# Optimization experiments

Measured on AMD Instinct MI355X. Metric: run time of the kernel, lower is better.

## Reference

```python
import jax, jax.numpy as jnp
import numpy as np

D_MODEL = 768
EXPAND = 2
D_INNER = EXPAND * D_MODEL  # 1536
D_STATE = 16
D_CONV = 4
DT_RANK = D_MODEL // 16  # 48
N_LAYER = 3
BATCH, SEQLEN = 2, 1024
EPS = 1e-5


def setup_inputs() -> dict:
    key = jax.random.key(0)
    ks = jax.random.split(key, 8)
    s = 0.02
    hidden_states = jax.random.normal(ks[0], (BATCH, SEQLEN, D_MODEL), jnp.float32)
    norm_w = jnp.ones((N_LAYER, D_MODEL), jnp.float32)
    in_proj_w = s * jax.random.normal(ks[1], (N_LAYER, 2 * D_INNER, D_MODEL), jnp.float32)
    conv_w = s * jax.random.normal(ks[2], (N_LAYER, D_INNER, D_CONV), jnp.float32)
    conv_b = jnp.zeros((N_LAYER, D_INNER), jnp.float32)
    x_proj_w = s * jax.random.normal(ks[3], (N_LAYER, DT_RANK + 2 * D_STATE, D_INNER), jnp.float32)
    dt_proj_w = s * jax.random.normal(ks[4], (N_LAYER, D_INNER, DT_RANK), jnp.float32)
    dt_proj_b = jnp.full((N_LAYER, D_INNER), -4.6, jnp.float32)  # softplus ~ 0.01
    # S4D-real init: A_log = log(1..d_state), tiled over channels
    A_log = jnp.tile(jnp.log(jnp.arange(1, D_STATE + 1, dtype=jnp.float32))[None, None, :], (N_LAYER, D_INNER, 1))
    D_skip = jnp.ones((N_LAYER, D_INNER), jnp.float32)
    out_proj_w = s * jax.random.normal(ks[5], (N_LAYER, D_MODEL, D_INNER), jnp.float32)
    norm_f_w = jnp.ones((D_MODEL,), jnp.float32)
    return dict(hidden_states=hidden_states, norm_w=norm_w, in_proj_w=in_proj_w,
                conv_w=conv_w, conv_b=conv_b, x_proj_w=x_proj_w, dt_proj_w=dt_proj_w,
                dt_proj_b=dt_proj_b, A_log=A_log, D_skip=D_skip, out_proj_w=out_proj_w,
                norm_f_w=norm_f_w)


def _rmsnorm(x, w):
    return x * jax.lax.rsqrt(jnp.mean(x * x, axis=-1, keepdims=True) + EPS) * w


def _causal_conv1d(x, w, b):
    # x: [B, L, D]; w: [D, K] depthwise; left-pad for causality
    xt = jnp.transpose(x, (0, 2, 1))  # [B, D, L]
    y = jax.lax.conv_general_dilated(xt, w[:, None, :], window_strides=(1,),
                                     padding=[(D_CONV - 1, 0)], feature_group_count=D_INNER)
    return jnp.transpose(y, (0, 2, 1)) + b


def _selective_scan(u, delta, A, Bc, Cc, Dp):
    # u, delta: [B, L, D]; A: [D, N]; Bc, Cc: [B, L, N]
    def step(h, inp):
        dt, bt, ct, ut = inp  # [B,D], [B,N], [B,N], [B,D]
        h = jnp.exp(dt[..., None] * A) * h + (dt * ut)[..., None] * bt[:, None, :]
        y = jnp.einsum('bdn,bn->bd', h, ct)
        return h, y
    h0 = jnp.zeros((u.shape[0], u.shape[2], A.shape[1]), u.dtype)
    xs = (jnp.swapaxes(delta, 0, 1), jnp.swapaxes(Bc, 0, 1), jnp.swapaxes(Cc, 0, 1), jnp.swapaxes(u, 0, 1))
    _, ys = jax.lax.scan(step, h0, xs)  # ys: [L, B, D]
    return jnp.swapaxes(ys, 0, 1) + u * Dp


def _mixer(h, in_w, cw, cb, xw, dtw, dtb, A_log, Dp, ow):
    xz = jnp.einsum('bld,ed->ble', h, in_w)  # [B, L, 2*D_INNER]
    x, z = xz[..., :D_INNER], xz[..., D_INNER:]
    x = jax.nn.silu(_causal_conv1d(x, cw, cb))
    x_dbl = jnp.einsum('bld,ed->ble', x, xw)
    dt = x_dbl[..., :DT_RANK]
    Bc = x_dbl[..., DT_RANK:DT_RANK + D_STATE]
    Cc = x_dbl[..., DT_RANK + D_STATE:]
    delta = jax.nn.softplus(jnp.einsum('blr,dr->bld', dt, dtw) + dtb)
    A = -jnp.exp(A_log)
    y = _selective_scan(x, delta, A, Bc, Cc, Dp)
    y = y * jax.nn.silu(z)
    return jnp.einsum('bld,ed->ble', y, ow)


def reference(hidden_states, norm_w, in_proj_w, conv_w, conv_b, x_proj_w, dt_proj_w,
              dt_proj_b, A_log, D_skip, out_proj_w, norm_f_w):
    hidden = hidden_states
    residual = None
    for i in range(N_LAYER):
        residual = hidden if residual is None else hidden + residual  # fused add
        hidden = _rmsnorm(residual, norm_w[i])
        hidden = _mixer(hidden, in_proj_w[i], conv_w[i], conv_b[i], x_proj_w[i],
                        dt_proj_w[i], dt_proj_b[i], A_log[i], D_skip[i], out_proj_w[i])
    # final fused add + RMSNorm (prenorm=False)
    return _rmsnorm(hidden + residual, norm_f_w)
```

## Files before the change

kernel.cpp:

```cpp
#include <hip/hip_runtime.h>
#include <math.h>

#define D_MODEL 768
#define D_INNER 1536
#define D_STATE 16
#define D_CONV 4
#define DT_RANK 48
#define N_LAYER 3
#define BATCH 2
#define SEQLEN 1024
#define NROWS (BATCH * SEQLEN)
#define XDBL_W (DT_RANK + 2 * D_STATE)
#define EPS 1e-5f

#define SCLEN 16
#define SDN 16
#define KSPLIT_X 8

typedef short bf16x8 __attribute__((ext_vector_type(8)));
typedef float f32x4 __attribute__((ext_vector_type(4)));

__device__ __forceinline__ ushort f2bf(float x) {
    union { float f; uint u; } v; v.f = x;
    uint r = v.u + 0x7fff + ((v.u >> 16) & 1);
    return (ushort)(r >> 16);
}

__device__ __forceinline__ void gload_lds16(const void* g, void* l) {
    __builtin_amdgcn_global_load_lds(
        (const __attribute__((address_space(1))) unsigned int*)g,
        (__attribute__((address_space(3))) unsigned int*)l, 16, 0, 0);
}

__global__ __launch_bounds__(256) void cvt_bf16_kernel(
    const float* __restrict__ s, ushort* __restrict__ d, int n4)
{
    int i = blockIdx.x * 256 + threadIdx.x;
    if (i >= n4) return;
    float4 v = ((const float4*)s)[i];
    ushort4 o;
    o.x = f2bf(v.x); o.y = f2bf(v.y); o.z = f2bf(v.z); o.w = f2bf(v.w);
    ((ushort4*)d)[i] = o;
}

__global__ __launch_bounds__(256) void cvt_xw_pad_kernel(
    const float* __restrict__ src, ushort* __restrict__ dst)
{
    const int per = 128 * 1536 / 4;
    int i = blockIdx.x * 256 + threadIdx.x;
    if (i >= 3 * per) return;
    int li = i / per, rem = i - li * per;
    int r = (rem * 4) / 1536, c = (rem * 4) % 1536;
    ushort4 o = make_ushort4(0, 0, 0, 0);
    if (r < XDBL_W) {
        const float* s = src + ((size_t)li * XDBL_W + r) * 1536 + c;
        o.x = f2bf(s[0]); o.y = f2bf(s[1]); o.z = f2bf(s[2]); o.w = f2bf(s[3]);
    }
    ((ushort4*)dst)[i] = o;
}

__global__ __launch_bounds__(256) void cvt_dtw_pad_kernel(
    const float* __restrict__ src, ushort* __restrict__ dst)
{
    const int per = 1536 * 64 / 4;
    int i = blockIdx.x * 256 + threadIdx.x;
    if (i >= 3 * per) return;
    int li = i / per, rem = i - li * per;
    int r = (rem * 4) / 64, c = (rem * 4) % 64;
    ushort4 o = make_ushort4(0, 0, 0, 0);
    if (c < DT_RANK) {
        const float* s = src + ((size_t)li * 1536 + r) * DT_RANK + c;
        o.x = f2bf(s[0]); o.y = f2bf(s[1]); o.z = f2bf(s[2]); o.w = f2bf(s[3]);
    }
    ((ushort4*)dst)[i] = o;
}

__global__ __launch_bounds__(256) void add_rmsnorm_kernel(
    const float* __restrict__ x, const float* __restrict__ res_in,
    const float* __restrict__ w, float* __restrict__ res_out,
    float* __restrict__ normed_f32, ushort* __restrict__ normed_bf)
{
    int row = blockIdx.x;
    int tid = threadIdx.x;
    const float* xr = x + row * D_MODEL;
    float v[3];
    float ss = 0.f;
#pragma unroll
    for (int i = 0; i < 3; i++) {
        int c = tid + i * 256;
        float t = xr[c];
        if (res_in) t += res_in[row * D_MODEL + c];
        v[i] = t;
        ss += t * t;
    }
    for (int off = 32; off; off >>= 1) ss += __shfl_xor(ss, off, 64);
    __shared__ float red[4];
    if ((tid & 63) == 0) red[tid >> 6] = ss;
    __syncthreads();
    float tot = red[0] + red[1] + red[2] + red[3];
    float scale = rsqrtf(tot * (1.f / D_MODEL) + EPS);
#pragma unroll
    for (int i = 0; i < 3; i++) {
        int c = tid + i * 256;
        if (res_out) res_out[row * D_MODEL + c] = v[i];
        float o = v[i] * scale * w[c];
        if (normed_f32) normed_f32[row * D_MODEL + c] = o;
        if (normed_bf)  normed_bf[row * D_MODEL + c] = f2bf(o);
    }
}

template <int BM, int BN, int EPI, int SPLITK>
__global__ __launch_bounds__(256) void gemm_mfma_kernel(
    const ushort* __restrict__ A, const ushort* __restrict__ W,
    const float* __restrict__ bias, float* __restrict__ C,
    int ldc, int Nout, int M, int K)
{
    constexpr int TM = BM / 32;
    constexpr int TN = BN / 32;
    __shared__ __attribute__((aligned(16))) ushort As[BM * 64];
    __shared__ __attribute__((aligned(16))) ushort Ws[BN * 64];
    const int t = threadIdx.x;
    const int lane = t & 63, w = t >> 6;
    const int ln15 = lane & 15, q = lane >> 4;
    const int row0 = blockIdx.y * BM, col0 = blockIdx.x * BN;
    const int wm0 = (w & 1) * (BM / 2), wn0 = (w >> 1) * (BN / 2);

    int kper = K / SPLITK;
    int kz = (SPLITK > 1) ? blockIdx.z * kper : 0;
    if (SPLITK > 1) C += (size_t)blockIdx.z * M * ldc;

    f32x4 acc[TM][TN];
#pragma unroll
    for (int i = 0; i < TM; i++)
#pragma unroll
        for (int j = 0; j < TN; j++) acc[i][j] = (f32x4){0.f, 0.f, 0.f, 0.f};

    for (int k0 = kz; k0 < kz + kper; k0 += 64) {
        __syncthreads();
#pragma unroll
        for (int i = 0; i < BM / 32; i++) {
            int p = (i * 4 + w) * 64 + lane;
            int r = p >> 3, s = p & 7;
            int g = s ^ (r & 7);
            gload_lds16(A + (size_t)(row0 + r) * K + k0 + g * 8, &As[p * 8]);
        }
#pragma unroll
        for (int i = 0; i < BN / 32; i++) {
            int p = (i * 4 + w) * 64 + lane;
            int r = p >> 3, s = p & 7;
            int g = s ^ (r & 7);
            gload_lds16(W + (size_t)(col0 + r) * K + k0 + g * 8, &Ws[p * 8]);
        }
        __syncthreads();
#pragma unroll
        for (int ks = 0; ks < 2; ks++) {
            bf16x8 af[TM], wf[TN];
#pragma unroll
            for (int im = 0; im < TM; im++) {
                int m = wm0 + im * 16 + ln15;
                int slot = (ks * 4 + q) ^ (m & 7);
                af[im] = *(const bf16x8*)&As[m * 64 + slot * 8];
            }
#pragma unroll
            for (int jn = 0; jn < TN; jn++) {
                int n = wn0 + jn * 16 + ln15;
                int slot = (ks * 4 + q) ^ (n & 7);
                wf[jn] = *(const bf16x8*)&Ws[n * 64 + slot * 8];
            }
#pragma unroll
            for (int im = 0; im < TM; im++)
#pragma unroll
                for (int jn = 0; jn < TN; jn++)
                    acc[im][jn] = __builtin_amdgcn_mfma_f32_16x16x32_bf16(
                        af[im], wf[jn], acc[im][jn], 0, 0, 0);
        }
    }
#pragma unroll
    for (int im = 0; im < TM; im++) {
#pragma unroll
        for (int jn = 0; jn < TN; jn++) {
            int rr = row0 + wm0 + im * 16 + q * 4;
            int cc = col0 + wn0 + jn * 16 + ln15;
            if (cc < Nout) {
                float* cp = C + (size_t)rr * ldc + cc;
#pragma unroll
                for (int r = 0; r < 4; r++) {
                    float v = acc[im][jn][r];
                    if (EPI == 1) {
                        v += bias[cc];
                        v = (v > 20.f) ? v : log1pf(__expf(v));
                    }
                    cp[(size_t)r * ldc] = v;
                }
            }
        }
    }
}

__global__ __launch_bounds__(256) void xreduce_kernel(
    const float* __restrict__ Cp, float* __restrict__ xdbl,
    ushort* __restrict__ xdt)
{
    const int S4 = NROWS * XDBL_W / 4;
    int i = blockIdx.x * 256 + threadIdx.x;
    if (i >= S4) return;
    const float4* p = (const float4*)Cp;
    float4 o = p[i];
#pragma unroll
    for (int z = 1; z < KSPLIT_X; z++) {
        float4 a = p[i + (size_t)z * S4];
        o.x += a.x; o.y += a.y; o.z += a.z; o.w += a.w;
    }
    ((float4*)xdbl)[i] = o;
    int row = (i * 4) / XDBL_W, c0 = (i * 4) % XDBL_W;
    if (c0 < DT_RANK) {
        ushort4 b;
        b.x = f2bf(o.x); b.y = f2bf(o.y); b.z = f2bf(o.z); b.w = f2bf(o.w);
        *(ushort4*)&xdt[(size_t)row * 64 + c0] = b;
    } else if (c0 < 64) {
        *(ushort4*)&xdt[(size_t)row * 64 + c0] = make_ushort4(0, 0, 0, 0);
    }
}

__global__ __launch_bounds__(256) void conv_silu_kernel(
    const float* __restrict__ xz, const float* __restrict__ cw,
    const float* __restrict__ cb, float* __restrict__ out,
    ushort* __restrict__ out_bf)
{
    int idx = blockIdx.x * 256 + threadIdx.x;
    int d = idx % D_INNER;
    int bl = idx / D_INNER;
    int l = bl % SEQLEN;
    float s = cb[d];
    const float* xp = xz + (size_t)bl * (2 * D_INNER) + d;
#pragma unroll
    for (int k = 0; k < D_CONV; k++) {
        int ls = l - (D_CONV - 1) + k;
        if (ls >= 0) s += cw[d * D_CONV + k] * xp[(k - (D_CONV - 1)) * (2 * D_INNER)];
    }
    float sil = s / (1.f + __expf(-s));
    out[(size_t)bl * D_INNER + d] = sil;
    out_bf[(size_t)bl * D_INNER + d] = f2bf(sil);
}

__global__ __launch_bounds__(1024) void scan2_kernel(
    const float* __restrict__ u, const float* __restrict__ delta,
    const float* __restrict__ A_log, const float* __restrict__ xdbl,
    const float* __restrict__ Dskip, const float* __restrict__ xz,
    ushort* __restrict__ ybf)
{
    __shared__ float PL[16][SDN * 17];
    __shared__ float HL[16][SDN * 17];
    const int t = threadIdx.x;
    const int lane = t & 63;
    const int w = t >> 6;
    const int dsub = lane & 15;
    const int csub = lane >> 4;
    const int c = w * 4 + csub;
    const int b = blockIdx.x / (D_INNER / SDN);
    const int d = (blockIdx.x % (D_INNER / SDN)) * SDN + dsub;

    float a2[D_STATE];
#pragma unroll
    for (int n = 0; n < D_STATE; n++)
        a2[n] = -__expf(A_log[d * D_STATE + n]) * 1.44269504f;

    const size_t base = (size_t)b * SEQLEN * D_INNER + d;
    const float* dtp = delta + base;
    const float* up  = u + base;
    const float* xrow = xdbl + (size_t)b * SEQLEN * XDBL_W;
    const int l0 = c * SCLEN;

    float h[D_STATE], P[D_STATE];
#pragma unroll
    for (int n = 0; n < D_STATE; n++) { h[n] = 0.f; P[n] = 1.f; }

    for (int i = 0; i < SCLEN; i++) {
        const int l = l0 + i;
        float dt = dtp[(size_t)l * D_INNER];
        float uu = up[(size_t)l * D_INNER];
        const float4* Bv = (const float4*)(xrow + (size_t)l * XDBL_W + DT_RANK);
        float4 q0 = Bv[0], q1 = Bv[1], q2 = Bv[2], q3 = Bv[3];
        float Bf[D_STATE] = {q0.x,q0.y,q0.z,q0.w, q1.x,q1.y,q1.z,q1.w,
                             q2.x,q2.y,q2.z,q2.w, q3.x,q3.y,q3.z,q3.w};
        float dtu = dt * uu;
#pragma unroll
        for (int n = 0; n < D_STATE; n++) {
            float e = __builtin_amdgcn_exp2f(dt * a2[n]);
            P[n] *= e;
            h[n] = e * h[n] + dtu * Bf[n];
        }
    }

#pragma unroll
    for (int n = 0; n < D_STATE; n++) {
        float Pp = __shfl(P[n], lane - 16, 64);
        float Hp = __shfl(h[n], lane - 16, 64);
        bool act = csub >= 1;
        h[n] = act ? P[n] * Hp + h[n] : h[n];
        P[n] = act ? P[n] * Pp : P[n];
    }
#pragma unroll
    for (int n = 0; n < D_STATE; n++) {
        float Pp = __shfl(P[n], lane - 32, 64);
        float Hp = __shfl(h[n], lane - 32, 64);
        bool act = csub >= 2;
        h[n] = act ? P[n] * Hp + h[n] : h[n];
        P[n] = act ? P[n] * Pp : P[n];
    }

    if (csub == 3) {
#pragma unroll
        for (int n = 0; n < D_STATE; n++) {
            PL[w][dsub * 17 + n] = P[n];
            HL[w][dsub * 17 + n] = h[n];
        }
    }
    __syncthreads();

    if (t < SDN * D_STATE) {
        const int d2 = t >> 4, n2 = t & 15;
        float hin = 0.f;
        for (int ww = 0; ww < 16; ww++) {
            float Pw = PL[ww][d2 * 17 + n2];
            float Hw = HL[ww][d2 * 17 + n2];
            HL[ww][d2 * 17 + n2] = hin;
            hin = Pw * hin + Hw;
        }
    }
    __syncthreads();

#pragma unroll
    for (int n = 0; n < D_STATE; n++) {
        float Win = HL[w][dsub * 17 + n];
        float Pe = __shfl(P[n], lane - 16, 64);
        float He = __shfl(h[n], lane - 16, 64);
        h[n] = (csub == 0) ? Win : Pe * Win + He;
    }

    const float Dsk = Dskip[d];
    const float* zp = xz + (size_t)b * SEQLEN * (2 * D_INNER) + D_INNER + d;
    ushort* yp = ybf + base;
    for (int i = 0; i < SCLEN; i++) {
        const int l = l0 + i;
        float dt = dtp[(size_t)l * D_INNER];
        float uu = up[(size_t)l * D_INNER];
        float zz = zp[(size_t)l * (2 * D_INNER)];
        const float4* Bv = (const float4*)(xrow + (size_t)l * XDBL_W + DT_RANK);
        float4 q0 = Bv[0], q1 = Bv[1], q2 = Bv[2], q3 = Bv[3];
        float4 r0 = Bv[4], r1 = Bv[5], r2 = Bv[6], r3 = Bv[7];
        float Bf[D_STATE] = {q0.x,q0.y,q0.z,q0.w, q1.x,q1.y,q1.z,q1.w,
                             q2.x,q2.y,q2.z,q2.w, q3.x,q3.y,q3.z,q3.w};
        float Cf[D_STATE] = {r0.x,r0.y,r0.z,r0.w, r1.x,r1.y,r1.z,r1.w,
                             r2.x,r2.y,r2.z,r2.w, r3.x,r3.y,r3.z,r3.w};
        float dtu = dt * uu;
        float acc = 0.f;
#pragma unroll
        for (int n = 0; n < D_STATE; n++) {
            float e = __builtin_amdgcn_exp2f(dt * a2[n]);
            h[n] = e * h[n] + dtu * Bf[n];
            acc += h[n] * Cf[n];
        }
        float yy = acc + uu * Dsk;
        float ee = __builtin_amdgcn_exp2f(-zz * 1.44269504f);
        float sil = zz * __builtin_amdgcn_rcpf(1.f + ee);
        yp[(size_t)l * D_INNER] = f2bf(yy * sil);
    }
}

extern "C" void kernel_launch(void* const* d_in, const int* in_sizes, int n_in,
                              void* d_out, int out_size, void* d_ws, size_t ws_size,
                              hipStream_t stream)
{
    const float* hs        = (const float*)d_in[0];
    const float* norm_w    = (const float*)d_in[1];
    const float* in_proj_w = (const float*)d_in[2];
    const float* conv_w    = (const float*)d_in[3];
    const float* conv_b    = (const float*)d_in[4];
    const float* x_proj_w  = (const float*)d_in[5];
    const float* dt_proj_w = (const float*)d_in[6];
    const float* dt_proj_b = (const float*)d_in[7];
    const float* A_log     = (const float*)d_in[8];
    const float* D_skip    = (const float*)d_in[9];
    const float* out_proj_w= (const float*)d_in[10];
    const float* norm_f_w  = (const float*)d_in[11];

    float* ws = (float*)d_ws;
    float* residual = ws;
    float* hidden   = residual + NROWS * D_MODEL;
    float* xz       = hidden + NROWS * D_MODEL;
    float* xconv    = xz + NROWS * 2 * D_INNER;
    float* xdbl     = xconv + NROWS * D_INNER;
    float* delta    = xdbl + NROWS * XDBL_W;
    float* xpart    = delta + NROWS * D_INNER;
    ushort* normbf  = (ushort*)(xpart + (size_t)KSPLIT_X * NROWS * XDBL_W);
    ushort* ybf     = normbf + NROWS * D_MODEL;
    ushort* xconvbf = ybf + NROWS * D_INNER;
    ushort* xdtbf   = xconvbf + NROWS * D_INNER;
    ushort* win_bf  = xdtbf + NROWS * 64;
    ushort* wout_bf = win_bf + (size_t)N_LAYER * 2 * D_INNER * D_MODEL;
    ushort* xw_pad  = wout_bf + (size_t)N_LAYER * D_MODEL * D_INNER;
    ushort* dtw_pad = xw_pad + (size_t)N_LAYER * 128 * 1536;

    {
        int n_in4  = N_LAYER * 2 * D_INNER * D_MODEL / 4;
        int n_out4 = N_LAYER * D_MODEL * D_INNER / 4;
        cvt_bf16_kernel<<<(n_in4 + 255) / 256, 256, 0, stream>>>(in_proj_w, win_bf, n_in4);
        cvt_bf16_kernel<<<(n_out4 + 255) / 256, 256, 0, stream>>>(out_proj_w, wout_bf, n_out4);
        cvt_xw_pad_kernel<<<(3 * 128 * 1536 / 4 + 255) / 256, 256, 0, stream>>>(x_proj_w, xw_pad);
        cvt_dtw_pad_kernel<<<(3 * 1536 * 64 / 4 + 255) / 256, 256, 0, stream>>>(dt_proj_w, dtw_pad);
    }

    for (int i = 0; i < N_LAYER; i++) {
        add_rmsnorm_kernel<<<NROWS, 256, 0, stream>>>(
            i == 0 ? hs : hidden, i == 0 ? nullptr : residual,
            norm_w + i * D_MODEL, residual, nullptr, normbf);
        gemm_mfma_kernel<64, 128, 0, 1><<<dim3(2 * D_INNER / 128, NROWS / 64), 256, 0, stream>>>(
            normbf, win_bf + (size_t)i * 2 * D_INNER * D_MODEL, nullptr,
            xz, 2 * D_INNER, 2 * D_INNER, NROWS, D_MODEL);
        conv_silu_kernel<<<NROWS * D_INNER / 256, 256, 0, stream>>>(
            xz, conv_w + i * D_INNER * D_CONV, conv_b + i * D_INNER, xconv, xconvbf);
        gemm_mfma_kernel<64, 128, 0, KSPLIT_X><<<dim3(1, NROWS / 64, KSPLIT_X), 256, 0, stream>>>(
            xconvbf, xw_pad + (size_t)i * 128 * 1536, nullptr,
            xpart, XDBL_W, XDBL_W, NROWS, D_INNER);
        xreduce_kernel<<<(NROWS * XDBL_W / 4 + 255) / 256, 256, 0, stream>>>(
            xpart, xdbl, xdtbf);
        gemm_mfma_kernel<128, 128, 1, 1><<<dim3(D_INNER / 128, NROWS / 128), 256, 0, stream>>>(
            xdtbf, dtw_pad + (size_t)i * 1536 * 64, dt_proj_b + i * D_INNER,
            delta, D_INNER, D_INNER, NROWS, 64);
        scan2_kernel<<<BATCH * (D_INNER / SDN), 1024, 0, stream>>>(
            xconv, delta, A_log + (size_t)i * D_INNER * D_STATE, xdbl,
            D_skip + i * D_INNER, xz, ybf);
        gemm_mfma_kernel<64, 64, 0, 1><<<dim3(D_MODEL / 64, NROWS / 64), 256, 0, stream>>>(
            ybf, wout_bf + (size_t)i * D_MODEL * D_INNER, nullptr,
            hidden, D_MODEL, D_MODEL, NROWS, D_INNER);
    }
    add_rmsnorm_kernel<<<NROWS, 256, 0, stream>>>(
        hidden, residual, norm_f_w, nullptr, (float*)d_out, nullptr);
}
```

Measured before the change: 497.9 us.

## Split selective scan into chunk-summary and apply passes; store xz in bf16

Replaces the single scan kernel (one 1024-thread block per batch and 16-channel group) with two kernels that also split the sequence into 4 quarters. The first kernel computes per-quarter decay/state summaries and the second combines the prior quarters' summaries before producing outputs. This raises block count from 192 to 768 for better occupancy on the GPU, at the cost of doing the recurrence twice. Separately, the in_proj GEMM now writes xz as bf16 to halve its traffic into conv and the gate read, and the dt_proj GEMM tile shrinks to 64 rows.

```diff
diff --git a/kernel.cpp b/kernel.cpp
--- a/kernel.cpp
+++ b/kernel.cpp
@@ -13,8 +13,11 @@
 #define XDBL_W (DT_RANK + 2 * D_STATE)
 #define EPS 1e-5f
 
-#define SCLEN 16
 #define SDN 16
+#define NDG (D_INNER / SDN)
+#define NSPLIT 4
+#define QSTEPS (SEQLEN / NSPLIT)
+#define SCLEN2 8
 #define KSPLIT_X 8
 
 typedef short bf16x8 __attribute__((ext_vector_type(8)));
@@ -24,6 +27,10 @@
     union { float f; uint u; } v; v.f = x;
     uint r = v.u + 0x7fff + ((v.u >> 16) & 1);
     return (ushort)(r >> 16);
+}
+__device__ __forceinline__ float bf2f(ushort x) {
+    union { uint u; float f; } v; v.u = ((uint)x) << 16;
+    return v.f;
 }
 
 __device__ __forceinline__ void gload_lds16(const void* g, void* l) {
@@ -109,10 +116,10 @@
     }
 }
 
-template <int BM, int BN, int EPI, int SPLITK>
+template <int BM, int BN, int EPI, int SPLITK, int OUTBF>
 __global__ __launch_bounds__(256) void gemm_mfma_kernel(
     const ushort* __restrict__ A, const ushort* __restrict__ W,
-    const float* __restrict__ bias, float* __restrict__ C,
+    const float* __restrict__ bias, void* __restrict__ Cv,
     int ldc, int Nout, int M, int K)
 {
     constexpr int TM = BM / 32;
@@ -127,7 +134,12 @@
 
     int kper = K / SPLITK;
     int kz = (SPLITK > 1) ? blockIdx.z * kper : 0;
-    if (SPLITK > 1) C += (size_t)blockIdx.z * M * ldc;
+    float* Cf = (float*)Cv;
+    ushort* Cb = (ushort*)Cv;
+    if (SPLITK > 1) {
+        Cf += (size_t)blockIdx.z * M * ldc;
+        Cb += (size_t)blockIdx.z * M * ldc;
+    }
 
     f32x4 acc[TM][TN];
 #pragma unroll
@@ -182,7 +194,6 @@
             int rr = row0 + wm0 + im * 16 + q * 4;
             int cc = col0 + wn0 + jn * 16 + ln15;
             if (cc < Nout) {
-                float* cp = C + (size_t)rr * ldc + cc;
 #pragma unroll
                 for (int r = 0; r < 4; r++) {
                     float v = acc[im][jn][r];
@@ -190,7 +201,8 @@
                         v += bias[cc];
                         v = (v > 20.f) ? v : log1pf(__expf(v));
                     }
-                    cp[(size_t)r * ldc] = v;
+                    if (OUTBF) Cb[(size_t)(rr + r) * ldc + cc] = f2bf(v);
+                    else       Cf[(size_t)(rr + r) * ldc + cc] = v;
                 }
             }
         }
@@ -223,7 +235,7 @@
 }
 
 __global__ __launch_bounds__(256) void conv_silu_kernel(
-    const float* __restrict__ xz, const float* __restrict__ cw,
+    const ushort* __restrict__ xzbf, const float* __restrict__ cw,
     const float* __restrict__ cb, float* __restrict__ out,
     ushort* __restrict__ out_bf)
 {
@@ -232,33 +244,37 @@
     int bl = idx / D_INNER;
     int l = bl % SEQLEN;
     float s = cb[d];
-    const float* xp = xz + (size_t)bl * (2 * D_INNER) + d;
+    const ushort* xp = xzbf + (size_t)bl * (2 * D_INNER) + d;
 #pragma unroll
     for (int k = 0; k < D_CONV; k++) {
         int ls = l - (D_CONV - 1) + k;
-        if (ls >= 0) s += cw[d * D_CONV + k] * xp[(k - (D_CONV - 1)) * (2 * D_INNER)];
+        if (ls >= 0) s += cw[d * D_CONV + k] * bf2f(xp[(k - (D_CONV - 1)) * (2 * D_INNER)]);
     }
     float sil = s / (1.f + __expf(-s));
     out[(size_t)bl * D_INNER + d] = sil;
     out_bf[(size_t)bl * D_INNER + d] = f2bf(sil);
 }
 
-__global__ __launch_bounds__(1024) void scan2_kernel(
+__global__ __launch_bounds__(512) void scanA_kernel(
     const float* __restrict__ u, const float* __restrict__ delta,
     const float* __restrict__ A_log, const float* __restrict__ xdbl,
-    const float* __restrict__ Dskip, const float* __restrict__ xz,
-    ushort* __restrict__ ybf)
-{
-    __shared__ float PL[16][SDN * 17];
-    __shared__ float HL[16][SDN * 17];
+    float* __restrict__ summ)
+{
+    __shared__ float PL[8][SDN * 17];
+    __shared__ float HL[8][SDN * 17];
     const int t = threadIdx.x;
     const int lane = t & 63;
     const int w = t >> 6;
     const int dsub = lane & 15;
     const int csub = lane >> 4;
+    const int bid = blockIdx.x;
+    const int qq = bid & 3;
+    const int rest = bid >> 2;
+    const int b = rest / NDG;
+    const int dg = rest % NDG;
+    const int d = dg * SDN + dsub;
     const int c = w * 4 + csub;
-    const int b = blockIdx.x / (D_INNER / SDN);
-    const int d = (blockIdx.x % (D_INNER / SDN)) * SDN + dsub;
+    const int l0 = qq * QSTEPS + c * SCLEN2;
 
     float a2[D_STATE];
 #pragma unroll
@@ -269,13 +285,12 @@
     const float* dtp = delta + base;
     const float* up  = u + base;
     const float* xrow = xdbl + (size_t)b * SEQLEN * XDBL_W;
-    const int l0 = c * SCLEN;
 
     float h[D_STATE], P[D_STATE];
 #pragma unroll
     for (int n = 0; n < D_STATE; n++) { h[n] = 0.f; P[n] = 1.f; }
 
-    for (int i = 0; i < SCLEN; i++) {
+    for (int i = 0; i < SCLEN2; i++) {
         const int l = l0 + i;
         float dt = dtp[(size_t)l * D_INNER];
         float uu = up[(size_t)l * D_INNER];
@@ -291,7 +306,6 @@
             h[n] = e * h[n] + dtu * Bf[n];
         }
     }
-
 #pragma unroll
     for (int n = 0; n < D_STATE; n++) {
         float Pp = __shfl(P[n], lane - 16, 64);
@@ -308,7 +322,6 @@
         h[n] = act ? P[n] * Hp + h[n] : h[n];
         P[n] = act ? P[n] * Pp : P[n];
     }
-
     if (csub == 3) {
 #pragma unroll
         for (int n = 0; n < D_STATE; n++) {
@@ -317,11 +330,111 @@
         }
     }
     __syncthreads();
-
     if (t < SDN * D_STATE) {
         const int d2 = t >> 4, n2 = t & 15;
+        float hin = 0.f, pin = 1.f;
+        for (int ww = 0; ww < 8; ww++) {
+            float Pw = PL[ww][d2 * 17 + n2];
+            float Hw = HL[ww][d2 * 17 + n2];
+            hin = Pw * hin + Hw;
+            pin *= Pw;
+        }
+        float* so = summ + ((size_t)rest * NSPLIT + qq) * 512;
+        so[t] = pin;
+        so[256 + t] = hin;
+    }
+}
+
+__global__ __launch_bounds__(512) void scanC_kernel(
+    const float* __restrict__ u, const float* __restrict__ delta,
+    const float* __restrict__ A_log, const float* __restrict__ xdbl,
+    const float* __restrict__ Dskip, const ushort* __restrict__ xzbf,
+    const float* __restrict__ summ, ushort* __restrict__ ybf)
+{
+    __shared__ float PL[8][SDN * 17];
+    __shared__ float HL[8][SDN * 17];
+    __shared__ float HIN[256];
+    const int t = threadIdx.x;
+    const int lane = t & 63;
+    const int w = t >> 6;
+    const int dsub = lane & 15;
+    const int csub = lane >> 4;
+    const int bid = blockIdx.x;
+    const int qq = bid & 3;
+    const int rest = bid >> 2;
+    const int b = rest / NDG;
+    const int dg = rest % NDG;
+    const int d = dg * SDN + dsub;
+    const int c = w * 4 + csub;
+    const int l0 = qq * QSTEPS + c * SCLEN2;
+
+    if (t < 256) {
         float hin = 0.f;
-        for (int ww = 0; ww < 16; ww++) {
+        for (int z = 0; z < qq; z++) {
+            const float* so = summ + ((size_t)rest * NSPLIT + z) * 512;
+            hin = so[t] * hin + so[256 + t];
+        }
+        HIN[t] = hin;
+    }
+
+    float a2[D_STATE];
+#pragma unroll
+    for (int n = 0; n < D_STATE; n++)
+        a2[n] = -__expf(A_log[d * D_STATE + n]) * 1.44269504f;
+
+    const size_t base = (size_t)b * SEQLEN * D_INNER + d;
+    const float* dtp = delta + base;
+    const float* up  = u + base;
+    const float* xrow = xdbl + (size_t)b * SEQLEN * XDBL_W;
+
+    float h[D_STATE], P[D_STATE];
+#pragma unroll
+    for (int n = 0; n < D_STATE; n++) { h[n] = 0.f; P[n] = 1.f; }
+
+    for (int i = 0; i < SCLEN2; i++) {
+        const int l = l0 + i;
+        float dt = dtp[(size_t)l * D_INNER];
+        float uu = up[(size_t)l * D_INNER];
+        const float4* Bv = (const float4*)(xrow + (size_t)l * XDBL_W + DT_RANK);
+        float4 q0 = Bv[0], q1 = Bv[1], q2 = Bv[2], q3 = Bv[3];
+        float Bf[D_STATE] = {q0.x,q0.y,q0.z,q0.w, q1.x,q1.y,q1.z,q1.w,
+                             q2.x,q2.y,q2.z,q2.w, q3.x,q3.y,q3.z,q3.w};
+        float dtu = dt * uu;
+#pragma unroll
+        for (int n = 0; n < D_STATE; n++) {
+            float e = __builtin_amdgcn_exp2f(dt * a2[n]);
+            P[n] *= e;
+            h[n] = e * h[n] + dtu * Bf[n];
+        }
+    }
+#pragma unroll
+    for (int n = 0; n < D_STATE; n++) {
+        float Pp = __shfl(P[n], lane - 16, 64);
+        float Hp = __shfl(h[n], lane - 16, 64);
+        bool act = csub >= 1;
+        h[n] = act ? P[n] * Hp + h[n] : h[n];
+        P[n] = act ? P[n] * Pp : P[n];
+    }
+#pragma unroll
+    for (int n = 0; n < D_STATE; n++) {
+        float Pp = __shfl(P[n], lane - 32, 64);
+        float Hp = __shfl(h[n], lane - 32, 64);
+        bool act = csub >= 2;
+        h[n] = act ? P[n] * Hp + h[n] : h[n];
+        P[n] = act ? P[n] * Pp : P[n];
+    }
+    if (csub == 3) {
+#pragma unroll
+        for (int n = 0; n < D_STATE; n++) {
+            PL[w][dsub * 17 + n] = P[n];
+            HL[w][dsub * 17 + n] = h[n];
+        }
+    }
+    __syncthreads();
+    if (t < SDN * D_STATE) {
+        const int d2 = t >> 4, n2 = t & 15;
+        float hin = HIN[t];
+        for (int ww = 0; ww < 8; ww++) {
             float Pw = PL[ww][d2 * 17 + n2];
             float Hw = HL[ww][d2 * 17 + n2];
             HL[ww][d2 * 17 + n2] = hin;
@@ -329,7 +442,6 @@
         }
     }
     __syncthreads();
-
 #pragma unroll
     for (int n = 0; n < D_STATE; n++) {
         float Win = HL[w][dsub * 17 + n];
@@ -337,15 +449,14 @@
         float He = __shfl(h[n], lane - 16, 64);
         h[n] = (csub == 0) ? Win : Pe * Win + He;
     }
-
     const float Dsk = Dskip[d];
-    const float* zp = xz + (size_t)b * SEQLEN * (2 * D_INNER) + D_INNER + d;
+    const ushort* zp = xzbf + (size_t)b * SEQLEN * (2 * D_INNER) + D_INNER + d;
     ushort* yp = ybf + base;
-    for (int i = 0; i < SCLEN; i++) {
+    for (int i = 0; i < SCLEN2; i++) {
         const int l = l0 + i;
         float dt = dtp[(size_t)l * D_INNER];
         float uu = up[(size_t)l * D_INNER];
-        float zz = zp[(size_t)l * (2 * D_INNER)];
+        float zz = bf2f(zp[(size_t)l * (2 * D_INNER)]);
         const float4* Bv = (const float4*)(xrow + (size_t)l * XDBL_W + DT_RANK);
         float4 q0 = Bv[0], q1 = Bv[1], q2 = Bv[2], q3 = Bv[3];
         float4 r0 = Bv[4], r1 = Bv[5], r2 = Bv[6], r3 = Bv[7];
@@ -388,12 +499,13 @@
     float* ws = (float*)d_ws;
     float* residual = ws;
     float* hidden   = residual + NROWS * D_MODEL;
-    float* xz       = hidden + NROWS * D_MODEL;
-    float* xconv    = xz + NROWS * 2 * D_INNER;
+    float* xconv    = hidden + NROWS * D_MODEL;
     float* xdbl     = xconv + NROWS * D_INNER;
     float* delta    = xdbl + NROWS * XDBL_W;
     float* xpart    = delta + NROWS * D_INNER;
-    ushort* normbf  = (ushort*)(xpart + (size_t)KSPLIT_X * NROWS * XDBL_W);
+    float* summ     = xpart + (size_t)KSPLIT_X * NROWS * XDBL_W;
+    ushort* xzbf    = (ushort*)(summ + (size_t)BATCH * NDG * NSPLIT * 512);
+    ushort* normbf  = xzbf + (size_t)NROWS * 2 * D_INNER;
     ushort* ybf     = normbf + NROWS * D_MODEL;
     ushort* xconvbf = ybf + NROWS * D_INNER;
     ushort* xdtbf   = xconvbf + NROWS * D_INNER;
@@ -415,23 +527,25 @@
         add_rmsnorm_kernel<<<NROWS, 256, 0, stream>>>(
             i == 0 ? hs : hidden, i == 0 ? nullptr : residual,
             norm_w + i * D_MODEL, residual, nullptr, normbf);
-        gemm_mfma_kernel<64, 128, 0, 1><<<dim3(2 * D_INNER / 128, NROWS / 64), 256, 0, stream>>>(
+        gemm_mfma_kernel<64, 128, 0, 1, 1><<<dim3(2 * D_INNER / 128, NROWS / 64), 256, 0, stream>>>(
             normbf, win_bf + (size_t)i * 2 * D_INNER * D_MODEL, nullptr,
-            xz, 2 * D_INNER, 2 * D_INNER, NROWS, D_MODEL);
+            xzbf, 2 * D_INNER, 2 * D_INNER, NROWS, D_MODEL);
         conv_silu_kernel<<<NROWS * D_INNER / 256, 256, 0, stream>>>(
-            xz, conv_w + i * D_INNER * D_CONV, conv_b + i * D_INNER, xconv, xconvbf);
-        gemm_mfma_kernel<64, 128, 0, KSPLIT_X><<<dim3(1, NROWS / 64, KSPLIT_X), 256, 0, stream>>>(
+            xzbf, conv_w + i * D_INNER * D_CONV, conv_b + i * D_INNER, xconv, xconvbf);
+        gemm_mfma_kernel<64, 128, 0, KSPLIT_X, 0><<<dim3(1, NROWS / 64, KSPLIT_X), 256, 0, stream>>>(
             xconvbf, xw_pad + (size_t)i * 128 * 1536, nullptr,
             xpart, XDBL_W, XDBL_W, NROWS, D_INNER);
         xreduce_kernel<<<(NROWS * XDBL_W / 4 + 255) / 256, 256, 0, stream>>>(
             xpart, xdbl, xdtbf);
-        gemm_mfma_kernel<128, 128, 1, 1><<<dim3(D_INNER / 128, NROWS / 128), 256, 0, stream>>>(
+        gemm_mfma_kernel<64, 128, 1, 1, 0><<<dim3(D_INNER / 128, NROWS / 64), 256, 0, stream>>>(
             xdtbf, dtw_pad + (size_t)i * 1536 * 64, dt_proj_b + i * D_INNER,
             delta, D_INNER, D_INNER, NROWS, 64);
-        scan2_kernel<<<BATCH * (D_INNER / SDN), 1024, 0, stream>>>(
+        scanA_kernel<<<BATCH * NDG * NSPLIT, 512, 0, stream>>>(
+            xconv, delta, A_log + (size_t)i * D_INNER * D_STATE, xdbl, summ);
+        scanC_kernel<<<BATCH * NDG * NSPLIT, 512, 0, stream>>>(
             xconv, delta, A_log + (size_t)i * D_INNER * D_STATE, xdbl,
-            D_skip + i * D_INNER, xz, ybf);
-        gemm_mfma_kernel<64, 64, 0, 1><<<dim3(D_MODEL / 64, NROWS / 64), 256, 0, stream>>>(
+            D_skip + i * D_INNER, xzbf, summ, ybf);
+        gemm_mfma_kernel<64, 64, 0, 1, 0><<<dim3(D_MODEL / 64, NROWS / 64), 256, 0, stream>>>(
             ybf, wout_bf + (size_t)i * D_MODEL * D_INNER, nullptr,
             hidden, D_MODEL, D_MODEL, NROWS, D_INNER);
     }
```

Result: slower. 510.5 us (+2.5%).
